# Kernel tuning notes

Hardware: AMD Instinct MI355X
Metric: run time of the kernel (lower is better)

The kernel has to match this reference:

```python
import jax, jax.numpy as jnp
import numpy as np
from jax import lax

# Module config (matches init_kwargs)
KH, KW = 2, 3          # kernel_size
C_IN = 64              # in_channels
C_HID = 256            # hidden_channels (4 * in_channels since in_channels <= 96)
C_OUT = 2 * C_IN       # affine transform -> (mu, log_scale)
DN = ('NCHW', 'OIHW', 'NCHW')


def setup_inputs() -> dict:
    key = jax.random.key(0)
    k0, k1, k2 = jax.random.split(key, 3)
    B, H, W = 32, 64, 64
    x = jax.random.normal(k0, (B, C_IN, H, W), dtype=jnp.float32)
    # masked (shifted) conv weights, order 'A' (height-causal)
    Wm = jax.random.normal(k1, (C_HID, C_IN, KH, KW), dtype=jnp.float32) * 0.05
    bm = jnp.zeros((C_HID,), dtype=jnp.float32)
    # 1x1 projection to transform params
    W1 = jax.random.normal(k2, (C_OUT, C_HID, 1, 1), dtype=jnp.float32) * 0.05
    b1 = jnp.zeros((C_OUT,), dtype=jnp.float32)
    return {"x": x, "Wm": Wm, "bm": bm, "W1": W1, "b1": b1}


def _mcf_block(x, Wm, bm, W1, b1):
    """MCFBlock: shifted masked conv (order 'A') -> ReLU -> 1x1 conv.

    Order 'A' causality: output at (h, w) depends only on input rows
    h-KH .. h-1 (strictly above) and columns w-(KW//2) .. w+(KW//2).
    Implemented by padding KH rows on top, (KW-1)//2 cols on each side,
    dropping the last row, then a VALID conv.
    """
    H = x.shape[2]
    cW = (KW - 1) // 2
    xp = jnp.pad(x, ((0, 0), (0, 0), (KH, 0), (cW, cW)))[:, :, :H + KH - 1]
    c = lax.conv_general_dilated(xp, Wm, (1, 1), 'VALID', dimension_numbers=DN)
    c = jax.nn.relu(c + bm[None, :, None, None])
    p = lax.conv_general_dilated(c, W1, (1, 1), 'VALID', dimension_numbers=DN)
    return p + b1[None, :, None, None]


def reference(x, Wm, bm, W1, b1):
    # params -> (mu, scale) for the affine flow (alpha = 1.0)
    params = _mcf_block(x, Wm, bm, W1, b1)      # [B, 2*C_IN, H, W]
    mu, log_scale = jnp.split(params, 2, axis=1)
    scale = jax.nn.sigmoid(log_scale + 2.0)     # macow affine parameterization
    out = scale * x + mu                        # [B, C_IN, H, W]
    logdet = jnp.sum(jnp.log(scale), axis=(1, 2, 3))  # [B]
    return out, logdet
```

## Files before the change

### kernel.cpp

```cpp
#include <hip/hip_runtime.h>
#include <math.h>


#define BATCH 32
#define HDIM 64
#define WDIM 64
#define ROWS 8
#define STRIPS 8
#define NBLK (BATCH * STRIPS)
#define NSLOT 10
#define CT_LD 264

typedef __attribute__((ext_vector_type(8))) short short8;
typedef __attribute__((ext_vector_type(4))) float f32x4;

__device__ inline unsigned short f2bf(float f) {
    union { float f; unsigned int u; } v; v.f = f;
    unsigned int u = v.u;
    unsigned int r = u + 0x7FFFu + ((u >> 16) & 1u);
    return (unsigned short)(r >> 16);
}

__device__ inline float bf2f(unsigned short s) {
    union { unsigned int u; float f; } v;
    v.u = ((unsigned int)s) << 16;
    return v.f;
}

__device__ inline int xt_off(int slot, int wp, int ci) {
    return ((slot * 66 + wp) << 6) + ((((ci >> 3) ^ (wp & 7)) << 3) | (ci & 7));
}

__global__ __launch_bounds__(256) void mcf_prep(
    const float* __restrict__ Wm, const float* __restrict__ W1,
    unsigned short* __restrict__ WmR, unsigned short* __restrict__ W1b)
{
    int idx = blockIdx.x * 256 + threadIdx.x;
    if (idx < 6 * 256 * 64) {
        int khkw = idx >> 14;
        int rem = idx & 16383;
        int co = rem >> 6;
        int ci = rem & 63;
        int kh = khkw / 3, kw = khkw % 3;
        WmR[idx] = f2bf(Wm[((co * 64 + ci) * 2 + kh) * 3 + kw]);
    } else {
        int i = idx - 6 * 256 * 64;
        W1b[i] = f2bf(W1[i]);
    }
}

__global__ __launch_bounds__(512, 2) void mcf_mfma(
    const float* __restrict__ x,
    const unsigned short* __restrict__ WmR,
    const float* __restrict__ bm,
    const unsigned short* __restrict__ W1b,
    const float* __restrict__ b1,
    float* __restrict__ out, float* __restrict__ row_ld)
{
    __shared__ __align__(16) unsigned short Xt[NSLOT * 66 * 64];
    __shared__ __align__(16) unsigned short Ct[2][64 * CT_LD];
    __shared__ float red[8];

    const int blk = blockIdx.x;
    const int b = blk >> 3;
    const int h0 = (blk & 7) * ROWS;
    const int tid = threadIdx.x;
    const int lane = tid & 63;
    const int wv = tid >> 6;
    const int col = lane & 15;
    const int g = lane >> 4;

    for (int l = tid; l < NSLOT * 128; l += 512) {
        int s = l >> 7, rr = l & 127;
        int wp = (rr >= 64) ? 65 : 0, ci = rr & 63;
        Xt[xt_off(s, wp, ci)] = 0;
    }
    #pragma unroll 4
    for (int it = 0; it < NSLOT * 4; ++it) {
        int idx = it * 512 + tid;
        int w = idx & 63;
        int ci = ((idx >> 6) & 31) * 2;
        int slot = idx >> 11;
        int row = h0 - 2 + slot;
        float v0 = 0.f, v1 = 0.f;
        if (row >= 0) {
            const float* base = &x[(((size_t)b * 64 + ci) * 64 + row) * 64 + w];
            v0 = base[0];
            v1 = base[64 * 64];
        }
        unsigned int pk = (unsigned int)f2bf(v0) | ((unsigned int)f2bf(v1) << 16);
        *reinterpret_cast<unsigned int*>(&Xt[xt_off(slot, w + 1, ci)]) = pk;
    }
    __syncthreads();

    float ldacc = 0.f;

    #pragma unroll 1
    for (int r = 0; r < ROWS; ++r) {
        unsigned short* Cb = Ct[r & 1];

        f32x4 acc[2][4];
        #pragma unroll
        for (int ct = 0; ct < 2; ++ct) {
            #pragma unroll
            for (int j = 0; j < 4; ++j) {
                float bv = bm[wv * 32 + ct * 16 + g * 4 + j];
                #pragma unroll
                for (int wt = 0; wt < 4; ++wt) acc[ct][wt][j] = bv;
            }
        }

        #pragma unroll
        for (int kh = 0; kh < 2; ++kh) {
            #pragma unroll
            for (int kw = 0; kw < 3; ++kw) {
                const unsigned short* wmk = WmR + ((kh * 3 + kw) << 14);
                #pragma unroll
                for (int ks = 0; ks < 2; ++ks) {
                    short8 bfrag[4];
                    #pragma unroll
                    for (int wt = 0; wt < 4; ++wt) {
                        int wp = wt * 16 + col + kw;
                        bfrag[wt] = *reinterpret_cast<const short8*>(
                            &Xt[(((r + kh) * 66 + wp) << 6) + ((((ks * 4 + g) ^ (wp & 7)) << 3))]);
                    }
                    #pragma unroll
                    for (int ct = 0; ct < 2; ++ct) {
                        short8 af = *reinterpret_cast<const short8*>(
                            &wmk[(wv * 32 + ct * 16 + col) * 64 + ks * 32 + g * 8]);
                        #pragma unroll
                        for (int wt = 0; wt < 4; ++wt)
                            acc[ct][wt] = __builtin_amdgcn_mfma_f32_16x16x32_bf16(
                                af, bfrag[wt], acc[ct][wt], 0, 0, 0);
                    }
                }
            }
        }
        #pragma unroll
        for (int ct = 0; ct < 2; ++ct) {
            int co_base = wv * 32 + ct * 16 + g * 4;
            #pragma unroll
            for (int wt = 0; wt < 4; ++wt) {
                int w = wt * 16 + col;
                unsigned short pk[4];
                #pragma unroll
                for (int j = 0; j < 4; ++j) pk[j] = f2bf(fmaxf(acc[ct][wt][j], 0.f));
                *reinterpret_cast<unsigned long long*>(&Cb[w * CT_LD + co_base]) =
                    *reinterpret_cast<const unsigned long long*>(pk);
            }
        }
        __syncthreads();

        {
            const int pr = wv & 3;
            const int wcg = wv >> 2;
            f32x4 accM[2], accL[2];
            #pragma unroll
            for (int j = 0; j < 4; ++j) {
                float bmu = b1[pr * 16 + g * 4 + j];
                float bls = b1[64 + pr * 16 + g * 4 + j];
                accM[0][j] = bmu; accM[1][j] = bmu;
                accL[0][j] = bls; accL[1][j] = bls;
            }
            #pragma unroll
            for (int ks = 0; ks < 8; ++ks) {
                int kk = ks * 32 + g * 8;
                short8 bf2[2];
                #pragma unroll
                for (int wt = 0; wt < 2; ++wt) {
                    int w = (wcg * 2 + wt) * 16 + col;
                    bf2[wt] = *reinterpret_cast<const short8*>(&Cb[w * CT_LD + kk]);
                }
                int oA = pr * 16 + col;
                short8 aM = *reinterpret_cast<const short8*>(&W1b[oA * 256 + kk]);
                short8 aL = *reinterpret_cast<const short8*>(&W1b[(oA + 64) * 256 + kk]);
                #pragma unroll
                for (int wt = 0; wt < 2; ++wt) {
                    accM[wt] = __builtin_amdgcn_mfma_f32_16x16x32_bf16(aM, bf2[wt], accM[wt], 0, 0, 0);
                    accL[wt] = __builtin_amdgcn_mfma_f32_16x16x32_bf16(aL, bf2[wt], accL[wt], 0, 0, 0);
                }
            }
            int h = h0 + r;
            float prod = 1.f;
            #pragma unroll
            for (int wt = 0; wt < 2; ++wt) {
                int w = (wcg * 2 + wt) * 16 + col;
                #pragma unroll
                for (int j = 0; j < 4; ++j) {
                    int co = pr * 16 + g * 4 + j;
                    float scale = 1.f / (1.f + __expf(-(accL[wt][j] + 2.f)));
                    float xv = bf2f(Xt[xt_off(r + 2, w + 1, co)]);
                    size_t xi = (((size_t)b * 64 + co) * 64 + h) * 64 + w;
                    out[xi] = scale * xv + accM[wt][j];
                    prod *= scale;
                }
            }
            ldacc += __logf(prod);
        }
    }

    #pragma unroll
    for (int off = 32; off; off >>= 1) ldacc += __shfl_down(ldacc, off);
    if (lane == 0) red[wv] = ldacc;
    __syncthreads();
    if (tid == 0) {
        float s = 0.f;
        #pragma unroll
        for (int i = 0; i < 8; ++i) s += red[i];
        row_ld[blk] = s;
    }
}

__global__ __launch_bounds__(64) void mcf_ldreduce(
    const float* __restrict__ row_ld, float* __restrict__ ldout)
{
    int b = blockIdx.x;
    int l = threadIdx.x;
    float v = (l < STRIPS) ? row_ld[b * STRIPS + l] : 0.f;
    #pragma unroll
    for (int off = 32; off; off >>= 1) v += __shfl_down(v, off);
    if (l == 0) ldout[b] = v;
}

extern "C" void kernel_launch(void* const* d_in, const int* in_sizes, int n_in,
                              void* d_out, int out_size, void* d_ws, size_t ws_size,
                              hipStream_t stream) {
    const float* x  = (const float*)d_in[0];
    const float* Wm = (const float*)d_in[1];
    const float* bm = (const float*)d_in[2];
    const float* W1 = (const float*)d_in[3];
    const float* b1 = (const float*)d_in[4];
    float* out = (float*)d_out;

    float* row_ld = (float*)d_ws;
    unsigned short* WmR = (unsigned short*)((char*)d_ws + 8192);
    unsigned short* W1b = WmR + 6 * 256 * 64;

    hipLaunchKernelGGL(mcf_prep, dim3(512), dim3(256), 0, stream,
                       Wm, W1, WmR, W1b);
    hipLaunchKernelGGL(mcf_mfma, dim3(NBLK), dim3(512), 0, stream,
                       x, WmR, bm, W1b, b1, out, row_ld);
    hipLaunchKernelGGL(mcf_ldreduce, dim3(BATCH), dim3(64), 0, stream,
                       row_ld, out + (size_t)BATCH * 64 * HDIM * WDIM);
}
```

Baseline: 65.60 us.

## Switch masked conv to 32x32x16 MFMA with per-wave 64co x 32w tiles

Replaces the 16x16x32 bf16 MFMA tiling of the masked conv (each wave 32 output channels x 64 columns) with 32x32x16 MFMAs, where each wave computes 64 channels x 32 columns. The bias is now added in the epilogue rather than used to initialise the accumulators. The LDS swizzle for the input tile gains an extra XOR bit so the new access pattern avoids bank conflicts. The aim is fewer LDS fragment loads per MFMA and better reuse of weight fragments. The cost is that weight loads from global now happen per ks with less column reuse.

```diff
diff --git a/kernel.cpp b/kernel.cpp
--- a/kernel.cpp
+++ b/kernel.cpp
@@ -13,6 +13,7 @@
 
 typedef __attribute__((ext_vector_type(8))) short short8;
 typedef __attribute__((ext_vector_type(4))) float f32x4;
+typedef __attribute__((ext_vector_type(16))) float f32x16;
 
 __device__ inline unsigned short f2bf(float f) {
     union { float f; unsigned int u; } v; v.f = f;
@@ -28,7 +29,8 @@
 }
 
 __device__ inline int xt_off(int slot, int wp, int ci) {
-    return ((slot * 66 + wp) << 6) + ((((ci >> 3) ^ (wp & 7)) << 3) | (ci & 7));
+    int chunk = (ci >> 3) ^ (wp & 7) ^ ((wp >> 3) & 1);
+    return ((slot * 66 + wp) << 6) + (chunk << 3) + (ci & 7);
 }
 
 __global__ __launch_bounds__(256) void mcf_prep(
@@ -69,6 +71,8 @@
     const int wv = tid >> 6;
     const int col = lane & 15;
     const int g = lane >> 4;
+    const int l31 = lane & 31;
+    const int l5 = lane >> 5;
 
     for (int l = tid; l < NSLOT * 128; l += 512) {
         int s = l >> 7, rr = l & 127;
@@ -93,22 +97,17 @@
     }
     __syncthreads();
 
+    const int cog = wv >> 1;
+    const int wtl = wv & 1;
     float ldacc = 0.f;
 
     #pragma unroll 1
     for (int r = 0; r < ROWS; ++r) {
         unsigned short* Cb = Ct[r & 1];
 
-        f32x4 acc[2][4];
+        f32x16 acc[2];
         #pragma unroll
-        for (int ct = 0; ct < 2; ++ct) {
-            #pragma unroll
-            for (int j = 0; j < 4; ++j) {
-                float bv = bm[wv * 32 + ct * 16 + g * 4 + j];
-                #pragma unroll
-                for (int wt = 0; wt < 4; ++wt) acc[ct][wt][j] = bv;
-            }
-        }
+        for (int j = 0; j < 16; ++j) { acc[0][j] = 0.f; acc[1][j] = 0.f; }
 
         #pragma unroll
         for (int kh = 0; kh < 2; ++kh) {
@@ -116,37 +115,37 @@
             for (int kw = 0; kw < 3; ++kw) {
                 const unsigned short* wmk = WmR + ((kh * 3 + kw) << 14);
                 #pragma unroll
-                for (int ks = 0; ks < 2; ++ks) {
-                    short8 bfrag[4];
+                for (int ks = 0; ks < 4; ++ks) {
+                    int wp = wtl * 32 + l31 + kw;
+                    int ci0 = ks * 16 + l5 * 8;
+                    short8 bfrag = *reinterpret_cast<const short8*>(
+                        &Xt[xt_off(r + kh, wp, ci0)]);
+                    short8 af0 = *reinterpret_cast<const short8*>(
+                        &wmk[(cog * 64 + l31) * 64 + ci0]);
+                    short8 af1 = *reinterpret_cast<const short8*>(
+                        &wmk[(cog * 64 + 32 + l31) * 64 + ci0]);
+                    acc[0] = __builtin_amdgcn_mfma_f32_32x32x16_bf16(
+                        af0, bfrag, acc[0], 0, 0, 0);
+                    acc[1] = __builtin_amdgcn_mfma_f32_32x32x16_bf16(
+                        af1, bfrag, acc[1], 0, 0, 0);
+                }
+            }
+        }
+        {
+            int w = wtl * 32 + l31;
+            #pragma unroll
+            for (int t = 0; t < 2; ++t) {
+                int cot = cog * 64 + t * 32;
+                #pragma unroll
+                for (int q = 0; q < 4; ++q) {
+                    int co = cot + q * 8 + 4 * l5;
+                    unsigned short pk[4];
                     #pragma unroll
-                    for (int wt = 0; wt < 4; ++wt) {
-                        int wp = wt * 16 + col + kw;
-                        bfrag[wt] = *reinterpret_cast<const short8*>(
-                            &Xt[(((r + kh) * 66 + wp) << 6) + ((((ks * 4 + g) ^ (wp & 7)) << 3))]);
-                    }
-                    #pragma unroll
-                    for (int ct = 0; ct < 2; ++ct) {
-                        short8 af = *reinterpret_cast<const short8*>(
-                            &wmk[(wv * 32 + ct * 16 + col) * 64 + ks * 32 + g * 8]);
-                        #pragma unroll
-                        for (int wt = 0; wt < 4; ++wt)
-                            acc[ct][wt] = __builtin_amdgcn_mfma_f32_16x16x32_bf16(
-                                af, bfrag[wt], acc[ct][wt], 0, 0, 0);
-                    }
-                }
-            }
-        }
-        #pragma unroll
-        for (int ct = 0; ct < 2; ++ct) {
-            int co_base = wv * 32 + ct * 16 + g * 4;
-            #pragma unroll
-            for (int wt = 0; wt < 4; ++wt) {
-                int w = wt * 16 + col;
-                unsigned short pk[4];
-                #pragma unroll
-                for (int j = 0; j < 4; ++j) pk[j] = f2bf(fmaxf(acc[ct][wt][j], 0.f));
-                *reinterpret_cast<unsigned long long*>(&Cb[w * CT_LD + co_base]) =
-                    *reinterpret_cast<const unsigned long long*>(pk);
+                    for (int j = 0; j < 4; ++j)
+                        pk[j] = f2bf(fmaxf(acc[t][q * 4 + j] + bm[co + j], 0.f));
+                    *reinterpret_cast<unsigned long long*>(&Cb[w * CT_LD + co]) =
+                        *reinterpret_cast<const unsigned long long*>(pk);
+                }
             }
         }
         __syncthreads();
```

Result: slower. 142.1 us (+116.5%).
